# Kernel optimization log

Hardware: AMD Instinct MI355X
Metric: run time of the kernel (lower is better)

The kernel has to match this reference:

```python
import jax, jax.numpy as jnp
import numpy as np

B_, L_, DM, DI, DS, DTR, DC = 1, 2048, 2048, 4096, 16, 128, 4


def setup_inputs() -> dict:
    key = jax.random.key(0)
    ks = jax.random.split(key, 8)
    s = lambda k, shape, scale: jax.random.normal(k, shape, jnp.float32) * scale
    inp = {
        "hidden_states": s(ks[0], (B_, L_, DM), 1.0),
        "in_proj_weight": s(ks[1], (2 * DI, DM), DM ** -0.5),
        "conv1d_weight": s(ks[2], (DI, 1, DC), DC ** -0.5),
        "x_proj_weight": s(ks[3], (DTR + 2 * DS, DI), DI ** -0.5),
        "dt_proj_weight": s(ks[4], (DI, DTR), DTR ** -0.5),
        "out_proj_weight": s(ks[5], (DM, DI), DI ** -0.5),
    }
    # dt_proj_bias = inverse-softplus of dt ~ LogUniform[1e-3, 0.1] (as in init_dtprojbias)
    dt = jnp.exp(jax.random.uniform(ks[6], (DI,), jnp.float32) * (np.log(0.1) - np.log(0.001)) + np.log(0.001))
    dt = jnp.clip(dt, 1e-4, None)
    inp["dt_proj_bias"] = dt + jnp.log(-jnp.expm1(-dt))
    # A_log init: log of repeat(arange(1, d_state+1)) per d_inner row
    inp["A_log"] = jnp.log(jnp.tile(jnp.arange(1, DS + 1, dtype=jnp.float32), (DI, 1)))
    inp["D"] = jnp.ones((DI,), jnp.float32)
    return inp


def reference(hidden_states, in_proj_weight, conv1d_weight, x_proj_weight,
              dt_proj_weight, dt_proj_bias, A_log, D, out_proj_weight):
    b, l, dm = hidden_states.shape
    di, ds = A_log.shape
    # in_proj: [b,l,dm] -> xz [b, 2*di, l]
    xz = jnp.einsum('ed,bld->bel', in_proj_weight, hidden_states)
    x, z = xz[:, :di], xz[:, di:]
    # depthwise causal conv1d (pad left d_conv-1, no bias) + SiLU
    x = jax.lax.conv_general_dilated(
        x, conv1d_weight, window_strides=(1,), padding=[(DC - 1, 0)],
        dimension_numbers=('NCH', 'OIH', 'NCH'), feature_group_count=di)
    x = jax.nn.silu(x)  # [b, di, l]
    # x_proj -> dt, B, C
    x_dbl = jnp.einsum('pd,bdl->blp', x_proj_weight, x)  # [b,l,dtr+2*ds]
    dt, Bc, Cc = jnp.split(x_dbl, [DTR, DTR + ds], axis=-1)
    delta = jnp.einsum('dr,blr->bld', dt_proj_weight, dt) + dt_proj_bias
    delta = jax.nn.softplus(delta)  # delta_softplus=True, delta_bias applied
    A = -jnp.exp(A_log)  # [di, ds]
    u = jnp.transpose(x, (0, 2, 1))  # [b,l,di]

    def step(h, inputs):
        d_t, B_t, C_t, u_t = inputs  # [b,di],[b,ds],[b,ds],[b,di]
        dA = jnp.exp(d_t[..., None] * A)                      # [b,di,ds]
        h = h * dA + (d_t * u_t)[..., None] * B_t[:, None, :]  # [b,di,ds]
        y = jnp.einsum('bdn,bn->bd', h, C_t)
        return h, y

    h0 = jnp.zeros((b, di, ds), hidden_states.dtype)
    xs = (jnp.swapaxes(delta, 0, 1), jnp.swapaxes(Bc, 0, 1),
          jnp.swapaxes(Cc, 0, 1), jnp.swapaxes(u, 0, 1))
    _, ys = jax.lax.scan(step, h0, xs)          # [l,b,di]
    y = jnp.swapaxes(ys, 0, 1) + u * D          # skip term u*D
    y = y * jax.nn.silu(jnp.transpose(z, (0, 2, 1)))  # gate
    return jnp.einsum('md,bld->blm', out_proj_weight, y)
```

## Files before the change

### kernel.cpp

```cpp
#include <hip/hip_runtime.h>
#include <hip/hip_bf16.h>

#define LSEQ 2048
#define DMODEL 2048
#define DINNER 4096
#define DSTATE 16
#define DTRANK 128
#define DCONV 4
#define DXP (DTRANK + 2*DSTATE)
#define NCHUNK 64
#define LCHUNK (LSEQ / NCHUNK)
#define KSPLIT 16
#define OKS 4

using bf16 = __hip_bfloat16;
typedef __attribute__((ext_vector_type(8))) short short8;
typedef __attribute__((ext_vector_type(4))) float float4v;

__device__ __forceinline__ float b2f(bf16 v) { return __bfloat162float(v); }
__device__ __forceinline__ bf16 f2b(float v) { return __float2bfloat16(v); }
__device__ __forceinline__ float bl16(unsigned u) { return __uint_as_float(u << 16); }
__device__ __forceinline__ float bh16(unsigned u) { return __uint_as_float(u & 0xffff0000u); }

__device__ __forceinline__ short f2bs(float v) {
    bf16 b = __float2bfloat16(v);
    union { bf16 b; short s; } u; u.b = b; return u.s;
}

__device__ __forceinline__ float fsilu(float x) {
    return x * __builtin_amdgcn_rcpf(1.0f + __expf(-x));
}

__device__ __forceinline__ short8 ld8(const float* p) {
    float4v f0 = *(const float4v*)p;
    float4v f1 = *(const float4v*)(p + 4);
    short8 r;
    r[0] = f2bs(f0[0]); r[1] = f2bs(f0[1]); r[2] = f2bs(f0[2]); r[3] = f2bs(f0[3]);
    r[4] = f2bs(f1[0]); r[5] = f2bs(f1[1]); r[6] = f2bs(f1[2]); r[7] = f2bs(f1[3]);
    return r;
}
__device__ __forceinline__ short8 ld8(const bf16* p) { return *(const short8*)p; }

template<typename CT> __device__ __forceinline__ CT cvtC(float v);
template<> __device__ __forceinline__ bf16  cvtC<bf16>(float v)  { return f2b(v); }
template<> __device__ __forceinline__ float cvtC<float>(float v) { return v; }

template<typename T> __device__ __forceinline__ float cvtL(T v);
template<> __device__ __forceinline__ float cvtL<bf16>(bf16 v)   { return b2f(v); }
template<> __device__ __forceinline__ float cvtL<float>(float v) { return v; }

__device__ __forceinline__ void glds16(const bf16* g, void* lds_base) {
    __builtin_amdgcn_global_load_lds(
        (const __attribute__((address_space(1))) void*)g,
        (__attribute__((address_space(3))) void*)lds_base, 16, 0, 0);
}

__global__ __launch_bounds__(256) void cvt3(
    const float* __restrict__ s0, bf16* __restrict__ d0, int n0,
    const float* __restrict__ s1, bf16* __restrict__ d1, int n1,
    const float* __restrict__ s2, bf16* __restrict__ d2, int n2)
{
    const int b = blockIdx.x;
    const int nb0 = n0 >> 11, nb1 = n1 >> 11;
    const float* s; bf16* d; int i;
    if (b < nb0)            { s = s0; d = d0; i = b * 2048; }
    else if (b < nb0 + nb1) { s = s1; d = d1; i = (b - nb0) * 2048; }
    else                    { s = s2; d = d2; i = (b - nb0 - nb1) * 2048; }
    i += threadIdx.x * 8;
    *(short8*)(d + i) = ld8(s + i);
}

__global__ __launch_bounds__(256) void cvt1(
    const float* __restrict__ src, bf16* __restrict__ dst, int n)
{
    int i = (blockIdx.x * 256 + threadIdx.x) * 8;
    if (i >= n) return;
    *(short8*)(dst + i) = ld8(src + i);
}

#define GBAR  __builtin_amdgcn_s_barrier()
#define VMW4  asm volatile("s_waitcnt vmcnt(4)" ::: "memory")
#define VMW0  asm volatile("s_waitcnt vmcnt(0)" ::: "memory")

#define LDA8(BASE, RB, AF) do {                                                \
  _Pragma("unroll") for (int mi_ = 0; mi_ < 4; ++mi_)                          \
  _Pragma("unroll") for (int kk_ = 0; kk_ < 2; ++kk_)                          \
    AF[mi_][kk_] = *(const short8*)((BASE) + (((RB) + mi_*16 + t16) << 6)      \
                                    + ((((kk_*4) + quad) ^ sw7) << 3));        \
} while (0)

#define LDB4(BASE, RB, BF) do {                                                \
  _Pragma("unroll") for (int nj_ = 0; nj_ < 2; ++nj_)                          \
  _Pragma("unroll") for (int kk_ = 0; kk_ < 2; ++kk_)                          \
    BF[nj_][kk_] = *(const short8*)((BASE) + (((RB) + nj_*16 + t16) << 6)      \
                                    + ((((kk_*4) + quad) ^ sw7) << 3));        \
} while (0)

#define MM16(AF, BF, MO, NO) do {                                              \
  _Pragma("unroll") for (int kk_ = 0; kk_ < 2; ++kk_)                          \
  _Pragma("unroll") for (int mi_ = 0; mi_ < 4; ++mi_)                          \
  _Pragma("unroll") for (int nj_ = 0; nj_ < 2; ++nj_)                          \
    acc[(MO)+mi_][(NO)+nj_] = __builtin_amdgcn_mfma_f32_16x16x32_bf16(         \
        AF[mi_][kk_], BF[nj_][kk_], acc[(MO)+mi_][(NO)+nj_], 0, 0, 0);         \
} while (0)

#define ST_ALO(tau) do { size_t ko_ = (size_t)(tau) << 6; int bo_ = ((tau)&1) << 15; \
  glds16(sA +       ko_, dA0 + bo_);                                           \
  glds16(sA + oA1 + ko_, dA1 + bo_); } while (0)
#define ST_AHI(tau) do { size_t ko_ = (size_t)(tau) << 6; int bo_ = ((tau)&1) << 15; \
  glds16(sA + oA2 + ko_, dA2 + bo_);                                           \
  glds16(sA + oA3 + ko_, dA3 + bo_); } while (0)
#define ST_BLO(tau) do { size_t ko_ = (size_t)(tau) << 6; int bo_ = ((tau)&1) << 15; \
  glds16(sB +       ko_, dB0 + bo_);                                           \
  glds16(sB + oB1 + ko_, dB1 + bo_); } while (0)
#define ST_BHI(tau) do { size_t ko_ = (size_t)(tau) << 6; int bo_ = ((tau)&1) << 15; \
  glds16(sB + oB2 + ko_, dB2 + bo_);                                           \
  glds16(sB + oB3 + ko_, dB3 + bo_); } while (0)

template<int NTI, bool SK>
__global__ __launch_bounds__(512, 2) void gemm_8ph(
    const bf16* __restrict__ A, int lda,
    const bf16* __restrict__ B, int ldb,
    void* __restrict__ Cout, int ldc, int Kc)
{
    __shared__ __align__(16) bf16 As[2][256 * 64];
    __shared__ __align__(16) bf16 Bs[2][256 * 64];

    const int t    = threadIdx.x;
    const int wave = t >> 6;
    const int lane = t & 63;
    const int t16  = lane & 15;
    const int quad = lane >> 4;
    const int sw7  = t16 & 7;
    const int wm   = (wave >> 2) * 128;
    const int wn   = (wave & 3) * 64;

    const int bid = blockIdx.x;
    const int s   = (bid & 7) * (gridDim.x >> 3) + (bid >> 3);
    const int bm0 = (s & 7) << 8;
    const int t2  = s >> 3;
    const int bn0 = (t2 & (NTI - 1)) << 8;
    const int ks  = t2 / NTI;

    const int lrow  = lane >> 3;
    const int lseg  = lane & 7;
    const int segx  = (lseg ^ lrow) * 8;
    const int bwoff = (wave & 3) * 8 + (wave >> 2) * 64;

    const bf16* sA = A + (size_t)(bm0 + wave * 8 + lrow) * lda + segx + (size_t)ks * Kc;
    const bf16* sB = B + (size_t)(bn0 + bwoff + lrow) * ldb + segx + (size_t)ks * Kc;
    const size_t oA1 = (size_t)128 * lda, oA2 = (size_t)64 * lda, oA3 = (size_t)192 * lda;
    const size_t oB1 = (size_t)128 * ldb, oB2 = (size_t)32 * ldb, oB3 = (size_t)160 * ldb;

    char* dA0 = (char*)&As[0][(  0 + wave * 8) * 64];
    char* dA1 = (char*)&As[0][(128 + wave * 8) * 64];
    char* dA2 = (char*)&As[0][( 64 + wave * 8) * 64];
    char* dA3 = (char*)&As[0][(192 + wave * 8) * 64];
    char* dB0 = (char*)&Bs[0][(  0 + bwoff) * 64];
    char* dB1 = (char*)&Bs[0][(128 + bwoff) * 64];
    char* dB2 = (char*)&Bs[0][( 32 + bwoff) * 64];
    char* dB3 = (char*)&Bs[0][(160 + bwoff) * 64];

    const int NT = Kc >> 6;

    float4v acc[8][4];
#pragma unroll
    for (int i = 0; i < 8; ++i)
#pragma unroll
        for (int j = 0; j < 4; ++j) acc[i][j] = (float4v)(0.0f);

    ST_ALO(0); ST_AHI(0); ST_BLO(0); ST_BHI(0);
    if (NT > 1) { ST_ALO(1); ST_BHI(1); VMW4; } else { VMW0; }
    GBAR;

    for (int T = 0; T < NT; ++T) {
        const bf16* Ab = As[T & 1];
        const bf16* Bb = Bs[T & 1];
        short8 af[4][2], b0[2][2], b1[2][2];

        LDA8(Ab, wm, af);
        LDB4(Bb, wn, b0);
        if (T + 1 < NT) { ST_AHI(T + 1); ST_BLO(T + 1); }
        __builtin_amdgcn_s_setprio(1);
        MM16(af, b0, 0, 0);
        __builtin_amdgcn_s_setprio(0);
        GBAR;

        LDB4(Bb, wn + 32, b1);
        if (T + 2 < NT) ST_ALO(T + 2);
        __builtin_amdgcn_s_setprio(1);
        MM16(af, b1, 0, 2);
        __builtin_amdgcn_s_setprio(0);
        GBAR;

        LDA8(Ab, wm + 64, af);
        if (T + 2 < NT) ST_BHI(T + 2);
        __builtin_amdgcn_s_setprio(1);
        MM16(af, b1, 4, 2);
        __builtin_amdgcn_s_setprio(0);
        GBAR;

        __builtin_amdgcn_s_setprio(1);
        MM16(af, b0, 4, 0);
        __builtin_amdgcn_s_setprio(0);
        if (T + 2 < NT) { VMW4; } else { VMW0; }
        GBAR;
    }

#pragma unroll
    for (int mi = 0; mi < 8; ++mi) {
#pragma unroll
        for (int nj = 0; nj < 4; ++nj) {
            const int m_base = bm0 + wm + (mi >> 2) * 64 + (mi & 3) * 16 + quad * 4;
            const int n_g    = bn0 + wn + (nj >> 1) * 32 + (nj & 1) * 16 + t16;
            if (SK) {
                float* P = (float*)Cout + (size_t)ks * 2048 * (size_t)ldc;
#pragma unroll
                for (int r = 0; r < 4; ++r)
                    P[(size_t)(m_base + r) * ldc + n_g] = acc[mi][nj][r];
            } else {
                bf16* C = (bf16*)Cout;
#pragma unroll
                for (int r = 0; r < 4; ++r)
                    C[(size_t)(m_base + r) * ldc + n_g] = f2b(acc[mi][nj][r]);
            }
        }
    }
}

__global__ __launch_bounds__(256) void reduce4f(
    const float* __restrict__ P, float* __restrict__ out, int MN)
{
    int i = (blockIdx.x * 256 + threadIdx.x) * 4;
    if (i >= MN) return;
    float4v s = *(const float4v*)(P + i);
#pragma unroll
    for (int ks = 1; ks < OKS; ++ks) {
        float4v v = *(const float4v*)(P + (size_t)ks * MN + i);
#pragma unroll
        for (int j = 0; j < 4; ++j) s[j] += v[j];
    }
    *(float4v*)(out + i) = s;
}

template<int BN, typename CT, bool SP>
__global__ __launch_bounds__(256) void gemm_glds64(
    const bf16* __restrict__ A, int lda,
    const bf16* __restrict__ B, int ldb,
    CT* __restrict__ C, int ldc,
    int K, const float* __restrict__ bias)
{
    constexpr int NJ  = BN / 32;
    constexpr int BGL = BN / 32;
    __shared__ bf16 As[128][64];
    __shared__ bf16 Bs[BN][64];

    const int t    = threadIdx.x;
    const int wave = t >> 6;
    const int lane = t & 63;
    const int t16  = lane & 15;
    const int quad = lane >> 4;
    const int wm   = (wave >> 1) * 64;
    const int wn   = (wave & 1) * (BN / 2);
    const int bm0  = blockIdx.x * 128;
    const int bn0  = blockIdx.y * BN;

    const int lrow = lane >> 3;
    const int gseg = (((lane & 7) ^ lrow) * 8);

    const bf16* Ag[4]; char* Ad[4];
#pragma unroll
    for (int g = 0; g < 4; g++) {
        Ag[g] = A + (size_t)(bm0 + wave * 32 + g * 8 + lrow) * lda + gseg;
        Ad[g] = (char*)As + (wave * 32 + g * 8) * 128;
    }
    const bf16* Bg[BGL]; char* Bd[BGL];
#pragma unroll
    for (int g = 0; g < BGL; g++) {
        int r = (BN == 128) ? (wave * 32 + g * 8) : (wave * 16 + g * 8);
        Bg[g] = B + (size_t)(bn0 + r + lrow) * ldb + gseg;
        Bd[g] = (char*)Bs + r * 128;
    }

    float4v acc[4][NJ];
#pragma unroll
    for (int i = 0; i < 4; i++)
#pragma unroll
        for (int j = 0; j < NJ; j++) acc[i][j] = (float4v)(0.0f);

    const int sw = t16 & 7;

    for (int k0 = 0; k0 < K; k0 += 64) {
        __syncthreads();
#pragma unroll
        for (int g = 0; g < 4; g++)   glds16(Ag[g] + k0, Ad[g]);
#pragma unroll
        for (int g = 0; g < BGL; g++) glds16(Bg[g] + k0, Bd[g]);
        __syncthreads();

#pragma unroll
        for (int kk = 0; kk < 2; kk++) {
            const int kso = ((kk * 4 + quad) ^ sw) * 8;
            short8 a[4], b[NJ];
#pragma unroll
            for (int mi = 0; mi < 4; mi++)
                a[mi] = *(const short8*)(&As[wm + mi * 16 + t16][kso]);
#pragma unroll
            for (int nj = 0; nj < NJ; nj++)
                b[nj] = *(const short8*)(&Bs[wn + nj * 16 + t16][kso]);
#pragma unroll
            for (int mi = 0; mi < 4; mi++)
#pragma unroll
                for (int nj = 0; nj < NJ; nj++)
                    acc[mi][nj] = __builtin_amdgcn_mfma_f32_16x16x32_bf16(
                        a[mi], b[nj], acc[mi][nj], 0, 0, 0);
        }
    }

#pragma unroll
    for (int mi = 0; mi < 4; mi++) {
#pragma unroll
        for (int nj = 0; nj < NJ; nj++) {
            int n_g = bn0 + wn + nj * 16 + t16;
            float bia = SP ? bias[n_g] : 0.0f;
#pragma unroll
            for (int r = 0; r < 4; r++) {
                int m_g = bm0 + wm + mi * 16 + quad * 4 + r;
                float v = acc[mi][nj][r];
                if (SP) {
                    float x = v + bia;
                    v = (x > 20.0f) ? x : __logf(1.0f + __expf(x));
                }
                C[(size_t)m_g * ldc + n_g] = cvtC<CT>(v);
            }
        }
    }
}

template<typename AT, typename CT, bool SP>
__global__ __launch_bounds__(256) void gemm_bt(
    const AT* __restrict__ A, int lda,
    const float* __restrict__ B, int ldb,
    CT* __restrict__ C, int ldc,
    int M, int N, int K,
    const float* __restrict__ bias)
{
    __shared__ bf16 As[64][40];
    __shared__ bf16 Bs[64][40];

    const int t    = threadIdx.x;
    const int bm0  = blockIdx.x * 64;
    const int bn0  = blockIdx.y * 64;
    const int row  = t >> 2;
    const int seg  = (t & 3) * 8;
    const int wave = t >> 6;
    const int lane = t & 63;
    const int wm   = (wave >> 1) * 32;
    const int wn   = (wave & 1) * 32;
    const int t16  = lane & 15;
    const int quad = lane >> 4;

    float4v acc[2][2];
#pragma unroll
    for (int i = 0; i < 2; i++)
#pragma unroll
        for (int j = 0; j < 2; j++) acc[i][j] = (float4v)(0.0f);

    const AT*    Aptr = A + (size_t)(bm0 + row) * lda + seg;
    const float* Bptr = B + (size_t)(bn0 + row) * ldb + seg;
    const bool a_ok = (bm0 + row) < M;
    const bool b_ok = (bn0 + row) < N;
    const short8 zero8 = (short8)(0);

    for (int k0 = 0; k0 < K; k0 += 32) {
        short8 av = a_ok ? ld8(Aptr + k0) : zero8;
        short8 bv = b_ok ? ld8(Bptr + k0) : zero8;
        __syncthreads();
        *(short8*)(&As[row][seg]) = av;
        *(short8*)(&Bs[row][seg]) = bv;
        __syncthreads();

        short8 a0 = *(const short8*)(&As[wm + t16][quad * 8]);
        short8 a1 = *(const short8*)(&As[wm + 16 + t16][quad * 8]);
        short8 b0 = *(const short8*)(&Bs[wn + t16][quad * 8]);
        short8 b1 = *(const short8*)(&Bs[wn + 16 + t16][quad * 8]);
        acc[0][0] = __builtin_amdgcn_mfma_f32_16x16x32_bf16(a0, b0, acc[0][0], 0, 0, 0);
        acc[0][1] = __builtin_amdgcn_mfma_f32_16x16x32_bf16(a0, b1, acc[0][1], 0, 0, 0);
        acc[1][0] = __builtin_amdgcn_mfma_f32_16x16x32_bf16(a1, b0, acc[1][0], 0, 0, 0);
        acc[1][1] = __builtin_amdgcn_mfma_f32_16x16x32_bf16(a1, b1, acc[1][1], 0, 0, 0);
    }

#pragma unroll
    for (int i = 0; i < 2; i++) {
#pragma unroll
        for (int j = 0; j < 2; j++) {
            int n_g = bn0 + wn + j * 16 + t16;
            if (n_g >= N) continue;
            float bia = SP ? bias[n_g] : 0.0f;
#pragma unroll
            for (int r = 0; r < 4; r++) {
                int m_g = bm0 + wm + i * 16 + quad * 4 + r;
                if (m_g >= M) continue;
                float v = acc[i][j][r];
                if (SP) {
                    float x = v + bia;
                    v = (x > 20.0f) ? x : log1pf(__expf(x));
                }
                C[(size_t)m_g * ldc + n_g] = cvtC<CT>(v);
            }
        }
    }
}

__global__ __launch_bounds__(256) void gemm_bt_splitk(
    const bf16* __restrict__ A, int lda,
    const float* __restrict__ B, int ldb,
    float* __restrict__ P,
    int M, int N, int K)
{
    __shared__ bf16 As[64][40];
    __shared__ bf16 Bs[64][40];

    const int t    = threadIdx.x;
    const int bm0  = blockIdx.x * 64;
    const int bn0  = blockIdx.y * 64;
    const int ks   = blockIdx.z;
    const int KS   = gridDim.z;
    const int kbeg = ks * (K / KS);
    const int kend = kbeg + (K / KS);
    const int row  = t >> 2;
    const int seg  = (t & 3) * 8;
    const int wave = t >> 6;
    const int lane = t & 63;
    const int wm   = (wave >> 1) * 32;
    const int wn   = (wave & 1) * 32;
    const int t16  = lane & 15;
    const int quad = lane >> 4;

    float4v acc[2][2];
#pragma unroll
    for (int i = 0; i < 2; i++)
#pragma unroll
        for (int j = 0; j < 2; j++) acc[i][j] = (float4v)(0.0f);

    const bf16*  Aptr = A + (size_t)(bm0 + row) * lda + seg;
    const float* Bptr = B + (size_t)(bn0 + row) * ldb + seg;
    const bool a_ok = (bm0 + row) < M;
    const bool b_ok = (bn0 + row) < N;
    const short8 zero8 = (short8)(0);

    for (int k0 = kbeg; k0 < kend; k0 += 32) {
        short8 av = a_ok ? ld8(Aptr + k0) : zero8;
        short8 bv = b_ok ? ld8(Bptr + k0) : zero8;
        __syncthreads();
        *(short8*)(&As[row][seg]) = av;
        *(short8*)(&Bs[row][seg]) = bv;
        __syncthreads();

        short8 a0 = *(const short8*)(&As[wm + t16][quad * 8]);
        short8 a1 = *(const short8*)(&As[wm + 16 + t16][quad * 8]);
        short8 b0 = *(const short8*)(&Bs[wn + t16][quad * 8]);
        short8 b1 = *(const short8*)(&Bs[wn + 16 + t16][quad * 8]);
        acc[0][0] = __builtin_amdgcn_mfma_f32_16x16x32_bf16(a0, b0, acc[0][0], 0, 0, 0);
        acc[0][1] = __builtin_amdgcn_mfma_f32_16x16x32_bf16(a0, b1, acc[0][1], 0, 0, 0);
        acc[1][0] = __builtin_amdgcn_mfma_f32_16x16x32_bf16(a1, b0, acc[1][0], 0, 0, 0);
        acc[1][1] = __builtin_amdgcn_mfma_f32_16x16x32_bf16(a1, b1, acc[1][1], 0, 0, 0);
    }

    float* Pk = P + (size_t)ks * M * N;
#pragma unroll
    for (int i = 0; i < 2; i++) {
#pragma unroll
        for (int j = 0; j < 2; j++) {
            int n_g = bn0 + wn + j * 16 + t16;
            if (n_g >= N) continue;
#pragma unroll
            for (int r = 0; r < 4; r++) {
                int m_g = bm0 + wm + i * 16 + quad * 4 + r;
                if (m_g >= M) continue;
                Pk[(size_t)m_g * N + n_g] = acc[i][j][r];
            }
        }
    }
}

__global__ __launch_bounds__(256) void reduce_splitk(
    const float* __restrict__ P, bf16* __restrict__ C, float* __restrict__ bc, int MN)
{
    int i = blockIdx.x * 256 + threadIdx.x;
    if (i >= MN) return;
    float s = 0.f;
#pragma unroll
    for (int ks = 0; ks < KSPLIT; ks++) s += P[(size_t)ks * MN + i];
    C[i] = f2b(s);
    int l = i / DXP;
    int p = i - l * DXP;
    if (p >= DTRANK) bc[l * 32 + (p - DTRANK)] = s;
}

__global__ __launch_bounds__(256) void conv_silu_par(
    const bf16* __restrict__ xz, const float* __restrict__ w, bf16* __restrict__ xc)
{
    const int d  = blockIdx.x * 256 + threadIdx.x;
    const int lc = blockIdx.y * 256;
    const float w0 = w[d * 4 + 0];
    const float w1 = w[d * 4 + 1];
    const float w2 = w[d * 4 + 2];
    const float w3 = w[d * 4 + 3];
    const size_t S = 2 * DINNER;
    const bf16* p = xz + d;
    float xm3 = 0.f, xm2 = 0.f, xm1 = 0.f;
    if (lc >= 3) {
        xm3 = b2f(p[(size_t)(lc - 3) * S]);
        xm2 = b2f(p[(size_t)(lc - 2) * S]);
        xm1 = b2f(p[(size_t)(lc - 1) * S]);
    }
    for (int l = lc; l < lc + 256; ++l) {
        float x0 = b2f(p[(size_t)l * S]);
        float a = w0 * xm3 + w1 * xm2 + w2 * xm1 + w3 * x0;
        xc[(size_t)l * DINNER + d] = f2b(fsilu(a));
        xm3 = xm2; xm2 = xm1; xm1 = x0;
    }
}

__global__ __launch_bounds__(256) void conv_silu_inplace(
    bf16* __restrict__ xz, const float* __restrict__ w)
{
    const int d = blockIdx.x * 256 + threadIdx.x;
    const float w0 = w[d * 4 + 0];
    const float w1 = w[d * 4 + 1];
    const float w2 = w[d * 4 + 2];
    const float w3 = w[d * 4 + 3];
    bf16* p = xz + d;
    const size_t S = 2 * DINNER;
    float xm3 = 0.f, xm2 = 0.f, xm1 = 0.f;
    for (int l = 0; l < LSEQ; l += 4) {
        float x0 = b2f(p[(size_t)(l + 0) * S]);
        float x1 = b2f(p[(size_t)(l + 1) * S]);
        float x2 = b2f(p[(size_t)(l + 2) * S]);
        float x3 = b2f(p[(size_t)(l + 3) * S]);
        float a0 = w0 * xm3 + w1 * xm2 + w2 * xm1 + w3 * x0;
        float a1 = w0 * xm2 + w1 * xm1 + w2 * x0  + w3 * x1;
        float a2 = w0 * xm1 + w1 * x0  + w2 * x1  + w3 * x2;
        float a3 = w0 * x0  + w1 * x1  + w2 * x2  + w3 * x3;
        p[(size_t)(l + 0) * S] = f2b(a0 / (1.0f + __expf(-a0)));
        p[(size_t)(l + 1) * S] = f2b(a1 / (1.0f + __expf(-a1)));
        p[(size_t)(l + 2) * S] = f2b(a2 / (1.0f + __expf(-a2)));
        p[(size_t)(l + 3) * S] = f2b(a3 / (1.0f + __expf(-a3)));
        xm3 = x1; xm2 = x2; xm1 = x3;
    }
}

__global__ __launch_bounds__(256) void scan_chunk1(
    const float* __restrict__ dlt, const bf16* __restrict__ xc,
    const float* __restrict__ bc, const float* __restrict__ A_log,
    float* __restrict__ hend, float* __restrict__ Pbuf)
{
    const int nh = threadIdx.x & 1;
    const int d  = blockIdx.x * 128 + (threadIdx.x >> 1);
    const int c  = blockIdx.y;

    float Ac[8];
    {
        const float* ap = A_log + d * DSTATE + nh * 8;
#pragma unroll
        for (int i = 0; i < 8; i++) Ac[i] = -__expf(ap[i]);
    }

    float h[8] = {0.f,0.f,0.f,0.f,0.f,0.f,0.f,0.f};
    float sdelta = 0.f;
    const float* pd = dlt + (size_t)c * LCHUNK * DINNER + d;
    const bf16*  pu = xc  + (size_t)c * LCHUNK * DINNER + d;
    const float* pb = bc  + (size_t)c * LCHUNK * 32 + nh * 8;

#pragma unroll 2
    for (int l = 0; l < LCHUNK; ++l) {
        const float delta = *pd;
        const float u     = b2f(*pu);
        float4v B0 = *(const float4v*)pb;
        float4v B1 = *(const float4v*)(pb + 4);
        const float du = delta * u;
        sdelta += delta;
#pragma unroll
        for (int i = 0; i < 8; i++) {
            float dA = __expf(delta * Ac[i]);
            float Bi = (i < 4) ? B0[i] : B1[i - 4];
            h[i] = h[i] * dA + du * Bi;
        }
        pd += DINNER; pu += DINNER; pb += 32;
    }

    size_t idx = ((size_t)c * DINNER + d) * DSTATE + nh * 8;
    float4v hv0, hv1, pv0, pv1;
#pragma unroll
    for (int i = 0; i < 4; i++) { hv0[i] = h[i]; hv1[i] = h[i + 4]; }
#pragma unroll
    for (int i = 0; i < 4; i++) { pv0[i] = __expf(sdelta * Ac[i]); pv1[i] = __expf(sdelta * Ac[i + 4]); }
    *(float4v*)(hend + idx)     = hv0;
    *(float4v*)(hend + idx + 4) = hv1;
    *(float4v*)(Pbuf + idx)     = pv0;
    *(float4v*)(Pbuf + idx + 4) = pv1;
}

__global__ __launch_bounds__(256) void scan_combine(
    float* __restrict__ hend, const float* __restrict__ Pbuf)
{
    const int dn = blockIdx.x * 256 + threadIdx.x;
    const size_t STR = (size_t)DINNER * DSTATE;
    float H = 0.f;
    size_t idx = dn;
    for (int c0 = 0; c0 < NCHUNK; c0 += 8) {
        float he[8], pp[8];
#pragma unroll
        for (int j = 0; j < 8; j++) {
            he[j] = hend[idx + (size_t)j * STR];
            pp[j] = Pbuf[idx + (size_t)j * STR];
        }
#pragma unroll
        for (int j = 0; j < 8; j++) {
            hend[idx + (size_t)j * STR] = H;
            H = he[j] + pp[j] * H;
        }
        idx += 8 * STR;
    }
}

__global__ __launch_bounds__(256) void scan_chunk2(
    const float* __restrict__ dlt, const bf16* __restrict__ xc,
    bf16* __restrict__ xz, const float* __restrict__ bc,
    const float* __restrict__ A_log, const float* __restrict__ Dp,
    const float* __restrict__ Hin)
{
    const int nh = threadIdx.x & 1;
    const int d  = blockIdx.x * 128 + (threadIdx.x >> 1);
    const int c  = blockIdx.y;

    float Ac[8];
    {
        const float* ap = A_log + d * DSTATE + nh * 8;
#pragma unroll
        for (int i = 0; i < 8; i++) Ac[i] = -__expf(ap[i]);
    }
    const float Dv = Dp[d];

    float h[8];
    {
        size_t idx = ((size_t)c * DINNER + d) * DSTATE + nh * 8;
        float4v h0 = *(const float4v*)(Hin + idx);
        float4v h1 = *(const float4v*)(Hin + idx + 4);
#pragma unroll
        for (int i = 0; i < 4; i++) { h[i] = h0[i]; h[i + 4] = h1[i]; }
    }

    const float* pd = dlt + (size_t)c * LCHUNK * DINNER + d;
    const bf16*  pu = xc  + (size_t)c * LCHUNK * DINNER + d;
    const float* pb = bc  + (size_t)c * LCHUNK * 32 + nh * 8;
    bf16*        pz = xz  + (size_t)c * LCHUNK * (2 * DINNER) + DINNER + d;

#pragma unroll 2
    for (int l = 0; l < LCHUNK; ++l) {
        const float delta = *pd;
        const float u     = b2f(*pu);
        float4v B0 = *(const float4v*)pb;
        float4v B1 = *(const float4v*)(pb + 4);
        float4v C0 = *(const float4v*)(pb + 16);
        float4v C1 = *(const float4v*)(pb + 20);
        const float du = delta * u;
        float yv = 0.f;
#pragma unroll
        for (int i = 0; i < 8; i++) {
            float dA = __expf(delta * Ac[i]);
            float Bi = (i < 4) ? B0[i] : B1[i - 4];
            float Ci = (i < 4) ? C0[i] : C1[i - 4];
            h[i] = h[i] * dA + du * Bi;
            yv += h[i] * Ci;
        }
        yv += __shfl_xor(yv, 1);
        yv += u * Dv;
        float z = b2f(*pz);
        yv *= fsilu(z);
        if (nh == 0) *pz = f2b(yv);
        pd += DINNER; pu += DINNER; pb += 32; pz += 2 * DINNER;
    }
}

template<typename DT>
__global__ __launch_bounds__(256) void scan_serial(
    const DT* __restrict__ dlt, bf16* __restrict__ xz,
    const bf16* __restrict__ xdbl,
    const float* __restrict__ A_log, const float* __restrict__ Dp)
{
    const int nq = threadIdx.x & 3;
    const int d  = blockIdx.x * 64 + (threadIdx.x >> 2);
    float Ac[4];
#pragma unroll
    for (int i = 0; i < 4; i++)
        Ac[i] = -__expf(A_log[d * DSTATE + nq * 4 + i]);
    const float Dv = Dp[d];
    float h[4] = {0.f, 0.f, 0.f, 0.f};
    for (int l = 0; l < LSEQ; ++l) {
        const float delta = cvtL<DT>(dlt[(size_t)l * DINNER + d]);
        const float u     = b2f(xz[(size_t)l * (2 * DINNER) + d]);
        const uint2 qb = *(const uint2*)(xdbl + (size_t)l * DXP + DTRANK + nq * 4);
        const uint2 qc = *(const uint2*)(xdbl + (size_t)l * DXP + DTRANK + DSTATE + nq * 4);
        float Bv[4] = { bl16(qb.x), bh16(qb.x), bl16(qb.y), bh16(qb.y) };
        float Cv[4] = { bl16(qc.x), bh16(qc.x), bl16(qc.y), bh16(qc.y) };
        const float du = delta * u;
        float yv = 0.f;
#pragma unroll
        for (int i = 0; i < 4; i++) {
            float dA = __expf(delta * Ac[i]);
            h[i] = h[i] * dA + du * Bv[i];
            yv += h[i] * Cv[i];
        }
        yv += __shfl_xor(yv, 1);
        yv += __shfl_xor(yv, 2);
        if (nq == 0) {
            yv += u * Dv;
            bf16* zp = xz + (size_t)l * (2 * DINNER) + DINNER + d;
            float z = b2f(*zp);
            yv *= z / (1.0f + __expf(-z));
            *zp = f2b(yv);
        }
    }
}

extern "C" void kernel_launch(void* const* d_in, const int* in_sizes, int n_in,
                              void* d_out, int out_size, void* d_ws, size_t ws_size,
                              hipStream_t stream)
{
    const float* hs      = (const float*)d_in[0];
    const float* w_in    = (const float*)d_in[1];
    const float* w_conv  = (const float*)d_in[2];
    const float* w_xproj = (const float*)d_in[3];
    const float* w_dt    = (const float*)d_in[4];
    const float *w_out, *b_dt, *A_log, *Dp;
    if (in_sizes[5] == DMODEL * DINNER) {
        w_out = (const float*)d_in[5];
        b_dt  = (const float*)d_in[6];
        A_log = (const float*)d_in[7];
        Dp    = (const float*)d_in[8];
    } else {
        b_dt  = (const float*)d_in[5];
        A_log = (const float*)d_in[6];
        Dp    = (const float*)d_in[7];
        w_out = (const float*)d_in[8];
    }
    float* out = (float*)d_out;

    const size_t SZ_XZ   = (size_t)LSEQ * 2 * DINNER * sizeof(bf16);
    const size_t SZ_XC   = (size_t)LSEQ * DINNER * sizeof(bf16);
    const size_t SZ_XDBL = (size_t)LSEQ * DXP * sizeof(bf16);
    const size_t SZ_DLTF = (size_t)LSEQ * DINNER * sizeof(float);
    const size_t SZ_HP   = (size_t)NCHUNK * DINNER * DSTATE * sizeof(float);
    const size_t SZ_BC   = (size_t)LSEQ * 32 * sizeof(float);

    char* p = (char*)d_ws;
    bf16* xz = (bf16*)p; p += SZ_XZ;

    const size_t need_fast = SZ_XZ + SZ_XC + SZ_XDBL + SZ_DLTF + 2 * SZ_HP + SZ_BC;
    const bool fast = ws_size >= need_fast;

    dim3 blk(256);

    if (fast) {
        bf16*  xc   = (bf16*)p;  p += SZ_XC;
        bf16*  xdbl = (bf16*)p;  p += SZ_XDBL;
        char*  hpr  = p;         p += SZ_DLTF;
        char*  dreg = p;
        float* dlt  = (float*)hpr;
        float* hend = (float*)dreg;
        float* Pbuf = (float*)(dreg + SZ_HP);
        float* bcb  = (float*)(dreg + 2 * SZ_HP);

        bf16*  w_in_b  = (bf16*)hpr;
        float* xp_part = (float*)hpr;
        bf16*  hs_b    = (bf16*)dreg;
        bf16*  w_dt_b  = (bf16*)(dreg + (size_t)LSEQ * DMODEL * sizeof(bf16));
        bf16*  w_out_b = (bf16*)xc;
        float* p_out   = (float*)hpr;

        {
            int n0 = 2 * DINNER * DMODEL, n1 = LSEQ * DMODEL, n2 = DINNER * DTRANK;
            cvt3<<<dim3((n0 + n1 + n2) / 2048), blk, 0, stream>>>(
                w_in, w_in_b, n0, hs, hs_b, n1, w_dt, w_dt_b, n2);
        }

        gemm_8ph<32, false><<<dim3(256), dim3(512), 0, stream>>>(
            hs_b, DMODEL, w_in_b, DMODEL, xz, 2*DINNER, DMODEL);

        conv_silu_par<<<dim3(DINNER/256, LSEQ/256), blk, 0, stream>>>(xz, w_conv, xc);

        gemm_bt_splitk<<<dim3(LSEQ/64, 3, KSPLIT), blk, 0, stream>>>(
            xc, DINNER, w_xproj, DINNER, xp_part, LSEQ, DXP, DINNER);
        reduce_splitk<<<dim3((LSEQ * DXP + 255) / 256), blk, 0, stream>>>(
            xp_part, xdbl, bcb, LSEQ * DXP);

        gemm_glds64<128, float, true><<<dim3(LSEQ/128, DINNER/128), blk, 0, stream>>>(
            xdbl, DXP, w_dt_b, DTRANK, dlt, DINNER, DTRANK, b_dt);

        scan_chunk1<<<dim3(DINNER/128, NCHUNK), blk, 0, stream>>>(
            dlt, xc, bcb, A_log, hend, Pbuf);
        scan_combine<<<dim3(DINNER*DSTATE/256), blk, 0, stream>>>(hend, Pbuf);
        scan_chunk2<<<dim3(DINNER/128, NCHUNK), blk, 0, stream>>>(
            dlt, xc, xz, bcb, A_log, Dp, hend);

        cvt1<<<dim3((DMODEL*DINNER)/2048), blk, 0, stream>>>(w_out, w_out_b, DMODEL*DINNER);
        gemm_8ph<8, true><<<dim3(256), dim3(512), 0, stream>>>(
            xz + DINNER, 2*DINNER, w_out_b, DINNER, p_out, DMODEL, DINNER/OKS);
        reduce4f<<<dim3(LSEQ*DMODEL/1024), blk, 0, stream>>>(
            p_out, out, LSEQ*DMODEL);
    } else {
        bf16* xdbl = (bf16*)p; p += SZ_XDBL;
        size_t used = (size_t)(p - (char*)d_ws);
        bool dlt_f32 = (ws_size - used) >= SZ_DLTF;

        gemm_bt<float, bf16, false><<<dim3(LSEQ/64, (2*DINNER)/64), blk, 0, stream>>>(
            hs, DMODEL, w_in, DMODEL, xz, 2*DINNER, LSEQ, 2*DINNER, DMODEL, nullptr);
        conv_silu_inplace<<<dim3(DINNER/256), blk, 0, stream>>>(xz, w_conv);
        gemm_bt<bf16, bf16, false><<<dim3(LSEQ/64, 3), blk, 0, stream>>>(
            xz, 2*DINNER, w_xproj, DINNER, xdbl, DXP, LSEQ, DXP, DINNER, nullptr);
        if (dlt_f32) {
            float* dlt = (float*)p;
            gemm_bt<bf16, float, true><<<dim3(LSEQ/64, DINNER/64), blk, 0, stream>>>(
                xdbl, DXP, w_dt, DTRANK, dlt, DINNER, LSEQ, DINNER, DTRANK, b_dt);
            scan_serial<float><<<dim3(DINNER/64), blk, 0, stream>>>(dlt, xz, xdbl, A_log, Dp);
        } else {
            bf16* dlt = (bf16*)p;
            gemm_bt<bf16, bf16, true><<<dim3(LSEQ/64, DINNER/64), blk, 0, stream>>>(
                xdbl, DXP, w_dt, DTRANK, dlt, DINNER, LSEQ, DINNER, DTRANK, b_dt);
            scan_serial<bf16><<<dim3(DINNER/64), blk, 0, stream>>>(dlt, xz, xdbl, A_log, Dp);
        }
        gemm_bt<bf16, float, false><<<dim3(LSEQ/64, DMODEL/64), blk, 0, stream>>>(
            xz + DINNER, 2*DINNER, w_out, DINNER, out, DMODEL, LSEQ, DMODEL, DINNER, nullptr);
    }
}
```

Before: 424.8 us.

## Unroll GEMM K-loop by two and give each scan thread all sixteen states

The 8-phase GEMM is split into dedicated in_proj and out_proj kernels. Each K-loop is manually unrolled by two, so LDS buffer indices become compile-time constants. The chunked scan kernels now assign one channel per thread with all 16 states, instead of two threads per channel with 8 states each. This removes the cross-lane shuffle, the redundant loads of delta, u and z, and the predicated store. The trade-off is half as many scan threads and blocks and more registers per thread, which can reduce latency hiding in the memory-bound scan.

```diff
diff --git a/kernel.cpp b/kernel.cpp
--- a/kernel.cpp
+++ b/kernel.cpp
@@ -117,49 +117,126 @@
   glds16(sB + oB2 + ko_, dB2 + bo_);                                           \
   glds16(sB + oB3 + ko_, dB3 + bo_); } while (0)
 
-template<int NTI, bool SK>
-__global__ __launch_bounds__(512, 2) void gemm_8ph(
+#define KSTEP(T, BI) do {                                                      \
+    const bf16* Ab = As[BI];                                                   \
+    const bf16* Bb = Bs[BI];                                                   \
+    short8 af[4][2], b0[2][2], b1[2][2];                                       \
+                                       \
+    LDA8(Ab, wm, af);                                                          \
+    LDB4(Bb, wn, b0);                                                          \
+    if ((T) + 1 < NT) { ST_AHI((T) + 1); ST_BLO((T) + 1); }                    \
+    __builtin_amdgcn_s_setprio(1); MM16(af, b0, 0, 0);                         \
+    __builtin_amdgcn_s_setprio(0); GBAR;                                       \
+                    \
+    LDB4(Bb, wn + 32, b1);                                                     \
+    if ((T) + 2 < NT) ST_ALO((T) + 2);                                         \
+    __builtin_amdgcn_s_setprio(1); MM16(af, b1, 0, 2);                         \
+    __builtin_amdgcn_s_setprio(0); GBAR;                                       \
+                           \
+    LDA8(Ab, wm + 64, af);                                                     \
+    if ((T) + 2 < NT) ST_BHI((T) + 2);                                         \
+    __builtin_amdgcn_s_setprio(1); MM16(af, b1, 4, 2);                         \
+    __builtin_amdgcn_s_setprio(0); GBAR;                                       \
+                                   \
+    __builtin_amdgcn_s_setprio(1); MM16(af, b0, 4, 0);                         \
+    __builtin_amdgcn_s_setprio(0);                                             \
+    if ((T) + 2 < NT) { VMW4; } else { VMW0; }                                 \
+    GBAR;                                                                      \
+} while (0)
+
+#define GEMM_PRO_COMMON                                                        \
+    const int t    = threadIdx.x;                                              \
+    const int wave = t >> 6;                                                   \
+    const int lane = t & 63;                                                   \
+    const int t16  = lane & 15;                                                \
+    const int quad = lane >> 4;                                                \
+    const int sw7  = t16 & 7;                                                  \
+    const int wm   = (wave >> 2) * 128;                                        \
+    const int wn   = (wave & 3) * 64;                                          \
+    const int lrow  = lane >> 3;                                               \
+    const int lseg  = lane & 7;                                                \
+    const int segx  = (lseg ^ lrow) * 8;                                       \
+    const int bwoff = (wave & 3) * 8 + (wave >> 2) * 64;
+
+#define GEMM_LDS_DSTS                                                          \
+    char* dA0 = (char*)&As[0][(  0 + wave * 8) * 64];                          \
+    char* dA1 = (char*)&As[0][(128 + wave * 8) * 64];                          \
+    char* dA2 = (char*)&As[0][( 64 + wave * 8) * 64];                          \
+    char* dA3 = (char*)&As[0][(192 + wave * 8) * 64];                          \
+    char* dB0 = (char*)&Bs[0][(  0 + bwoff) * 64];                             \
+    char* dB1 = (char*)&Bs[0][(128 + bwoff) * 64];                             \
+    char* dB2 = (char*)&Bs[0][( 32 + bwoff) * 64];                             \
+    char* dB3 = (char*)&Bs[0][(160 + bwoff) * 64];
+
+__global__ __launch_bounds__(512, 2) void gemm_inproj(
     const bf16* __restrict__ A, int lda,
     const bf16* __restrict__ B, int ldb,
-    void* __restrict__ Cout, int ldc, int Kc)
+    bf16* __restrict__ C, int ldc, int K)
 {
     __shared__ __align__(16) bf16 As[2][256 * 64];
     __shared__ __align__(16) bf16 Bs[2][256 * 64];
-
-    const int t    = threadIdx.x;
-    const int wave = t >> 6;
-    const int lane = t & 63;
-    const int t16  = lane & 15;
-    const int quad = lane >> 4;
-    const int sw7  = t16 & 7;
-    const int wm   = (wave >> 2) * 128;
-    const int wn   = (wave & 3) * 64;
-
+    GEMM_PRO_COMMON
+    const int bid = blockIdx.x;
+    const int s   = (bid & 7) * (gridDim.x >> 3) + (bid >> 3);
+    const int bm0 = (s & 7) << 8;
+    const int bn0 = (s >> 3) << 8;
+
+    const bf16* sA = A + (size_t)(bm0 + wave * 8 + lrow) * lda + segx;
+    const bf16* sB = B + (size_t)(bn0 + bwoff + lrow) * ldb + segx;
+    const size_t oA1 = (size_t)128 * lda, oA2 = (size_t)64 * lda, oA3 = (size_t)192 * lda;
+    const size_t oB1 = (size_t)128 * ldb, oB2 = (size_t)32 * ldb, oB3 = (size_t)160 * ldb;
+    GEMM_LDS_DSTS
+
+    const int NT = K >> 6;
+
+    float4v acc[8][4];
+#pragma unroll
+    for (int i = 0; i < 8; ++i)
+#pragma unroll
+        for (int j = 0; j < 4; ++j) acc[i][j] = (float4v)(0.0f);
+
+    ST_ALO(0); ST_AHI(0); ST_BLO(0); ST_BHI(0);
+    if (NT > 1) { ST_ALO(1); ST_BHI(1); VMW4; } else { VMW0; }
+    GBAR;
+
+    for (int T = 0; T < NT; T += 2) {
+        KSTEP(T, 0);
+        KSTEP(T + 1, 1);
+    }
+
+#pragma unroll
+    for (int mi = 0; mi < 8; ++mi) {
+#pragma unroll
+        for (int nj = 0; nj < 4; ++nj) {
+            const int m_base = bm0 + wm + (mi >> 2) * 64 + (mi & 3) * 16 + quad * 4;
+            const int n_g    = bn0 + wn + (nj >> 1) * 32 + (nj & 1) * 16 + t16;
+#pragma unroll
+            for (int r = 0; r < 4; ++r)
+                C[(size_t)(m_base + r) * ldc + n_g] = f2b(acc[mi][nj][r]);
+        }
+    }
+}
+
+__global__ __launch_bounds__(512, 2) void gemm_outproj(
+    const bf16* __restrict__ A, int lda,
+    const bf16* __restrict__ B, int ldb,
+    float* __restrict__ P, int ldc, int Kc)
+{
+    __shared__ __align__(16) bf16 As[2][256 * 64];
+    __shared__ __align__(16) bf16 Bs[2][256 * 64];
+    GEMM_PRO_COMMON
     const int bid = blockIdx.x;
     const int s   = (bid & 7) * (gridDim.x >> 3) + (bid >> 3);
     const int bm0 = (s & 7) << 8;
     const int t2  = s >> 3;
-    const int bn0 = (t2 & (NTI - 1)) << 8;
-    const int ks  = t2 / NTI;
-
-    const int lrow  = lane >> 3;
-    const int lseg  = lane & 7;
-    const int segx  = (lseg ^ lrow) * 8;
-    const int bwoff = (wave & 3) * 8 + (wave >> 2) * 64;
+    const int bn0 = (t2 & 7) << 8;
+    const int ks  = t2 >> 3;
 
     const bf16* sA = A + (size_t)(bm0 + wave * 8 + lrow) * lda + segx + (size_t)ks * Kc;
     const bf16* sB = B + (size_t)(bn0 + bwoff + lrow) * ldb + segx + (size_t)ks * Kc;
     const size_t oA1 = (size_t)128 * lda, oA2 = (size_t)64 * lda, oA3 = (size_t)192 * lda;
     const size_t oB1 = (size_t)128 * ldb, oB2 = (size_t)32 * ldb, oB3 = (size_t)160 * ldb;
-
-    char* dA0 = (char*)&As[0][(  0 + wave * 8) * 64];
-    char* dA1 = (char*)&As[0][(128 + wave * 8) * 64];
-    char* dA2 = (char*)&As[0][( 64 + wave * 8) * 64];
-    char* dA3 = (char*)&As[0][(192 + wave * 8) * 64];
-    char* dB0 = (char*)&Bs[0][(  0 + bwoff) * 64];
-    char* dB1 = (char*)&Bs[0][(128 + bwoff) * 64];
-    char* dB2 = (char*)&Bs[0][( 32 + bwoff) * 64];
-    char* dB3 = (char*)&Bs[0][(160 + bwoff) * 64];
+    GEMM_LDS_DSTS
 
     const int NT = Kc >> 6;
 
@@ -173,57 +250,21 @@
     if (NT > 1) { ST_ALO(1); ST_BHI(1); VMW4; } else { VMW0; }
     GBAR;
 
-    for (int T = 0; T < NT; ++T) {
-        const bf16* Ab = As[T & 1];
-        const bf16* Bb = Bs[T & 1];
-        short8 af[4][2], b0[2][2], b1[2][2];
-
-        LDA8(Ab, wm, af);
-        LDB4(Bb, wn, b0);
-        if (T + 1 < NT) { ST_AHI(T + 1); ST_BLO(T + 1); }
-        __builtin_amdgcn_s_setprio(1);
-        MM16(af, b0, 0, 0);
-        __builtin_amdgcn_s_setprio(0);
-        GBAR;
-
-        LDB4(Bb, wn + 32, b1);
-        if (T + 2 < NT) ST_ALO(T + 2);
-        __builtin_amdgcn_s_setprio(1);
-        MM16(af, b1, 0, 2);
-        __builtin_amdgcn_s_setprio(0);
-        GBAR;
-
-        LDA8(Ab, wm + 64, af);
-        if (T + 2 < NT) ST_BHI(T + 2);
-        __builtin_amdgcn_s_setprio(1);
-        MM16(af, b1, 4, 2);
-        __builtin_amdgcn_s_setprio(0);
-        GBAR;
-
-        __builtin_amdgcn_s_setprio(1);
-        MM16(af, b0, 4, 0);
-        __builtin_amdgcn_s_setprio(0);
-        if (T + 2 < NT) { VMW4; } else { VMW0; }
-        GBAR;
-    }
-
+    for (int T = 0; T < NT; T += 2) {
+        KSTEP(T, 0);
+        KSTEP(T + 1, 1);
+    }
+
+    float* Pk = P + (size_t)ks * 2048 * (size_t)ldc;
 #pragma unroll
     for (int mi = 0; mi < 8; ++mi) {
 #pragma unroll
         for (int nj = 0; nj < 4; ++nj) {
             const int m_base = bm0 + wm + (mi >> 2) * 64 + (mi & 3) * 16 + quad * 4;
             const int n_g    = bn0 + wn + (nj >> 1) * 32 + (nj & 1) * 16 + t16;
-            if (SK) {
-                float* P = (float*)Cout + (size_t)ks * 2048 * (size_t)ldc;
-#pragma unroll
-                for (int r = 0; r < 4; ++r)
-                    P[(size_t)(m_base + r) * ldc + n_g] = acc[mi][nj][r];
-            } else {
-                bf16* C = (bf16*)Cout;
-#pragma unroll
-                for (int r = 0; r < 4; ++r)
-                    C[(size_t)(m_base + r) * ldc + n_g] = f2b(acc[mi][nj][r]);
-            }
+#pragma unroll
+            for (int r = 0; r < 4; ++r)
+                Pk[(size_t)(m_base + r) * ldc + n_g] = acc[mi][nj][r];
         }
     }
 }
@@ -556,50 +597,57 @@
     const float* __restrict__ bc, const float* __restrict__ A_log,
     float* __restrict__ hend, float* __restrict__ Pbuf)
 {
-    const int nh = threadIdx.x & 1;
-    const int d  = blockIdx.x * 128 + (threadIdx.x >> 1);
-    const int c  = blockIdx.y;
-
-    float Ac[8];
+    const int d = blockIdx.x * 256 + threadIdx.x;
+    const int c = blockIdx.y;
+
+    float Ac[16];
     {
-        const float* ap = A_log + d * DSTATE + nh * 8;
-#pragma unroll
-        for (int i = 0; i < 8; i++) Ac[i] = -__expf(ap[i]);
-    }
-
-    float h[8] = {0.f,0.f,0.f,0.f,0.f,0.f,0.f,0.f};
+        const float* ap = A_log + d * DSTATE;
+#pragma unroll
+        for (int i = 0; i < 16; i++) Ac[i] = -__expf(ap[i]);
+    }
+
+    float h[16];
+#pragma unroll
+    for (int i = 0; i < 16; i++) h[i] = 0.f;
     float sdelta = 0.f;
+
     const float* pd = dlt + (size_t)c * LCHUNK * DINNER + d;
     const bf16*  pu = xc  + (size_t)c * LCHUNK * DINNER + d;
-    const float* pb = bc  + (size_t)c * LCHUNK * 32 + nh * 8;
+    const float* pb = bc  + (size_t)c * LCHUNK * 32;
 
 #pragma unroll 2
     for (int l = 0; l < LCHUNK; ++l) {
         const float delta = *pd;
         const float u     = b2f(*pu);
+        const float du    = delta * u;
+        sdelta += delta;
         float4v B0 = *(const float4v*)pb;
         float4v B1 = *(const float4v*)(pb + 4);
-        const float du = delta * u;
-        sdelta += delta;
-#pragma unroll
-        for (int i = 0; i < 8; i++) {
+        float4v B2 = *(const float4v*)(pb + 8);
+        float4v B3 = *(const float4v*)(pb + 12);
+#pragma unroll
+        for (int i = 0; i < 16; i++) {
             float dA = __expf(delta * Ac[i]);
-            float Bi = (i < 4) ? B0[i] : B1[i - 4];
+            float Bi = (i < 4) ? B0[i] : (i < 8) ? B1[i - 4] : (i < 12) ? B2[i - 8] : B3[i - 12];
             h[i] = h[i] * dA + du * Bi;
         }
         pd += DINNER; pu += DINNER; pb += 32;
     }
 
-    size_t idx = ((size_t)c * DINNER + d) * DSTATE + nh * 8;
-    float4v hv0, hv1, pv0, pv1;
-#pragma unroll
-    for (int i = 0; i < 4; i++) { hv0[i] = h[i]; hv1[i] = h[i + 4]; }
-#pragma unroll
-    for (int i = 0; i < 4; i++) { pv0[i] = __expf(sdelta * Ac[i]); pv1[i] = __expf(sdelta * Ac[i + 4]); }
-    *(float4v*)(hend + idx)     = hv0;
-    *(float4v*)(hend + idx + 4) = hv1;
-    *(float4v*)(Pbuf + idx)     = pv0;
-    *(float4v*)(Pbuf + idx + 4) = pv1;
+    float* hp = hend + ((size_t)c * DINNER + d) * DSTATE;
+    float* pp = Pbuf + ((size_t)c * DINNER + d) * DSTATE;
+#pragma unroll
+    for (int q = 0; q < 4; q++) {
+        float4v hv, pv;
+#pragma unroll
+        for (int j = 0; j < 4; j++) {
+            hv[j] = h[q * 4 + j];
+            pv[j] = __expf(sdelta * Ac[q * 4 + j]);
+        }
+        *(float4v*)(hp + q * 4) = hv;
+        *(float4v*)(pp + q * 4) = pv;
+    }
 }
 
 __global__ __launch_bounds__(256) void scan_combine(
@@ -631,55 +679,59 @@
     const float* __restrict__ A_log, const float* __restrict__ Dp,
     const float* __restrict__ Hin)
 {
-    const int nh = threadIdx.x & 1;
-    const int d  = blockIdx.x * 128 + (threadIdx.x >> 1);
-    const int c  = blockIdx.y;
-
-    float Ac[8];
+    const int d = blockIdx.x * 256 + threadIdx.x;
+    const int c = blockIdx.y;
+
+    float Ac[16];
     {
-        const float* ap = A_log + d * DSTATE + nh * 8;
-#pragma unroll
-        for (int i = 0; i < 8; i++) Ac[i] = -__expf(ap[i]);
+        const float* ap = A_log + d * DSTATE;
+#pragma unroll
+        for (int i = 0; i < 16; i++) Ac[i] = -__expf(ap[i]);
     }
     const float Dv = Dp[d];
 
-    float h[8];
+    float h[16];
     {
-        size_t idx = ((size_t)c * DINNER + d) * DSTATE + nh * 8;
-        float4v h0 = *(const float4v*)(Hin + idx);
-        float4v h1 = *(const float4v*)(Hin + idx + 4);
-#pragma unroll
-        for (int i = 0; i < 4; i++) { h[i] = h0[i]; h[i + 4] = h1[i]; }
+        const float* hp = Hin + ((size_t)c * DINNER + d) * DSTATE;
+#pragma unroll
+        for (int q = 0; q < 4; q++) {
+            float4v hv = *(const float4v*)(hp + q * 4);
+#pragma unroll
+            for (int j = 0; j < 4; j++) h[q * 4 + j] = hv[j];
+        }
     }
 
     const float* pd = dlt + (size_t)c * LCHUNK * DINNER + d;
     const bf16*  pu = xc  + (size_t)c * LCHUNK * DINNER + d;
-    const float* pb = bc  + (size_t)c * LCHUNK * 32 + nh * 8;
+    const float* pb = bc  + (size_t)c * LCHUNK * 32;
     bf16*        pz = xz  + (size_t)c * LCHUNK * (2 * DINNER) + DINNER + d;
 
 #pragma unroll 2
     for (int l = 0; l < LCHUNK; ++l) {
         const float delta = *pd;
         const float u     = b2f(*pu);
+        const float du    = delta * u;
         float4v B0 = *(const float4v*)pb;
         float4v B1 = *(const float4v*)(pb + 4);
+        float4v B2 = *(const float4v*)(pb + 8);
+        float4v B3 = *(const float4v*)(pb + 12);
         float4v C0 = *(const float4v*)(pb + 16);
         float4v C1 = *(const float4v*)(pb + 20);
-        const float du = delta * u;
+        float4v C2 = *(const float4v*)(pb + 24);
+        float4v C3 = *(const float4v*)(pb + 28);
         float yv = 0.f;
 #pragma unroll
-        for (int i = 0; i < 8; i++) {
+        for (int i = 0; i < 16; i++) {
             float dA = __expf(delta * Ac[i]);
-            float Bi = (i < 4) ? B0[i] : B1[i - 4];
-            float Ci = (i < 4) ? C0[i] : C1[i - 4];
+            float Bi = (i < 4) ? B0[i] : (i < 8) ? B1[i - 4] : (i < 12) ? B2[i - 8] : B3[i - 12];
+            float Ci = (i < 4) ? C0[i] : (i < 8) ? C1[i - 4] : (i < 12) ? C2[i - 8] : C3[i - 12];
             h[i] = h[i] * dA + du * Bi;
             yv += h[i] * Ci;
         }
-        yv += __shfl_xor(yv, 1);
         yv += u * Dv;
         float z = b2f(*pz);
         yv *= fsilu(z);
-        if (nh == 0) *pz = f2b(yv);
+        *pz = f2b(yv);
         pd += DINNER; pu += DINNER; pb += 32; pz += 2 * DINNER;
     }
 }
@@ -786,7 +838,7 @@
                 w_in, w_in_b, n0, hs, hs_b, n1, w_dt, w_dt_b, n2);
         }
 
-        gemm_8ph<32, false><<<dim3(256), dim3(512), 0, stream>>>(
+        gemm_inproj<<<dim3(256), dim3(512), 0, stream>>>(
             hs_b, DMODEL, w_in_b, DMODEL, xz, 2*DINNER, DMODEL);
 
         conv_silu_par<<<dim3(DINNER/256, LSEQ/256), blk, 0, stream>>>(xz, w_conv, xc);
@@ -799,14 +851,14 @@
         gemm_glds64<128, float, true><<<dim3(LSEQ/128, DINNER/128), blk, 0, stream>>>(
             xdbl, DXP, w_dt_b, DTRANK, dlt, DINNER, DTRANK, b_dt);
 
-        scan_chunk1<<<dim3(DINNER/128, NCHUNK), blk, 0, stream>>>(
+        scan_chunk1<<<dim3(DINNER/256, NCHUNK), blk, 0, stream>>>(
             dlt, xc, bcb, A_log, hend, Pbuf);
         scan_combine<<<dim3(DINNER*DSTATE/256), blk, 0, stream>>>(hend, Pbuf);
-        scan_chunk2<<<dim3(DINNER/128, NCHUNK), blk, 0, stream>>>(
+        scan_chunk2<<<dim3(DINNER/256, NCHUNK), blk, 0, stream>>>(
             dlt, xc, xz, bcb, A_log, Dp, hend);
 
         cvt1<<<dim3((DMODEL*DINNER)/2048), blk, 0, stream>>>(w_out, w_out_b, DMODEL*DINNER);
-        gemm_8ph<8, true><<<dim3(256), dim3(512), 0, stream>>>(
+        gemm_outproj<<<dim3(256), dim3(512), 0, stream>>>(
             xz + DINNER, 2*DINNER, w_out_b, DINNER, p_out, DMODEL, DINNER/OKS);
         reduce4f<<<dim3(LSEQ*DMODEL/1024), blk, 0, stream>>>(
             p_out, out, LSEQ*DMODEL);
```

After: 425.8 us. About the same (+0.2%).
